# Performance work log

Measured on AMD Instinct MI355X. Metric: run time of the kernel, lower is better.

The kernel has to match this reference:

```python
import jax, jax.numpy as jnp
import numpy as np

B, DIN, H1, H2 = 16384, 512, 256, 128
S, DC, DE, T, TE, GH = 4, 4, 2, 3, 2, 64
NDOM = DC * DE            # 8 domain experts total
ETOT = S + NDOM + TE      # 14 experts feeding each task gate


def setup_inputs() -> dict:
    key = jax.random.key(0)
    ks = jax.random.split(key, 20)
    w = lambda k, shape, fan: (jax.random.normal(k, shape, jnp.float32) / np.sqrt(fan).astype(np.float32))
    x = jax.random.normal(ks[0], (B, DIN), jnp.float32)
    domain_ids = jax.random.randint(ks[1], (B,), 0, DC, jnp.int64) if jax.config.jax_enable_x64 else jax.random.randint(ks[1], (B,), 0, DC, jnp.int32)
    return {
        "x": x,
        "domain_ids": domain_ids,
        # shared experts (stacked): input->256->128, ReLU on both layers
        "sW1": w(ks[2], (S, DIN, H1), DIN), "sb1": jnp.zeros((S, H1), jnp.float32),
        "sW2": w(ks[3], (S, H1, H2), H1),   "sb2": jnp.zeros((S, H2), jnp.float32),
        # domain experts, all domains stacked in order domain0..domainDC-1
        "dW1": w(ks[4], (NDOM, DIN, H1), DIN), "db1": jnp.zeros((NDOM, H1), jnp.float32),
        "dW2": w(ks[5], (NDOM, H1, H2), H1),   "db2": jnp.zeros((NDOM, H2), jnp.float32),
        # task experts, all tasks stacked task0..taskT-1
        "tW1": w(ks[6], (T * TE, DIN, H1), DIN), "tb1": jnp.zeros((T * TE, H1), jnp.float32),
        "tW2": w(ks[7], (T * TE, H1, H2), H1),   "tb2": jnp.zeros((T * TE, H2), jnp.float32),
        # task gates (stacked over tasks): input->64 (ReLU) -> ETOT (linear) -> softmax
        "gW1": w(ks[8], (T, DIN, GH), DIN), "gb1": jnp.zeros((T, GH), jnp.float32),
        "gW2": w(ks[9], (T, GH, ETOT), GH), "gb2": jnp.zeros((T, ETOT), jnp.float32),
    }


def _experts(x, W1, b1, W2, b2):
    # x: [B, DIN]; W1: [E, DIN, H1]; W2: [E, H1, H2] -> [B, E, H2]
    h = jax.nn.relu(jnp.einsum('bi,eih->beh', x, W1) + b1)
    return jax.nn.relu(jnp.einsum('beh,eho->beo', h, W2) + b2)


def reference(x, domain_ids, sW1, sb1, sW2, sb2, dW1, db1, dW2, db2,
              tW1, tb1, tW2, tb2, gW1, gb1, gW2, gb2):
    shared = _experts(x, sW1, sb1, sW2, sb2)          # [B, S, H2]
    domain = _experts(x, dW1, db1, dW2, db2)          # [B, NDOM, H2]
    task = _experts(x, tW1, tb1, tW2, tb2)            # [B, T*TE, H2]
    task = task.reshape(B, T, TE, H2)
    base = jnp.concatenate([shared, domain], axis=1)  # [B, S+NDOM, H2]
    base = jnp.broadcast_to(base[:, None], (B, T, S + NDOM, H2))
    all_experts = jnp.concatenate([base, task], axis=2)  # [B, T, ETOT, H2]
    # task gates
    gh = jax.nn.relu(jnp.einsum('bi,tig->btg', x, gW1) + gb1)
    gates = jax.nn.softmax(jnp.einsum('btg,tge->bte', gh, gW2) + gb2, axis=-1)  # [B, T, ETOT]
    out = jnp.einsum('bteh,bte->tbh', all_experts, gates)  # [T, B, H2]
    # note: the torch per-sample domain_weighted_output is computed then discarded;
    # only these task outputs are returned, and they do not depend on domain_ids.
    return tuple(out[t] for t in range(T))
```

## Files before the change

### kernel.cpp

```cpp
#include <hip/hip_runtime.h>
#include <hip/hip_bf16.h>

#define NB 16384
#define DIN 512
#define H1 256
#define H2 128
#define NE 18
#define NT 3
#define NGH 64
#define NETOT 14

typedef float f32x4 __attribute__((ext_vector_type(4)));
typedef short s16x8 __attribute__((ext_vector_type(8)));
typedef unsigned short u16;
typedef unsigned int u32;

__device__ __forceinline__ u16 f2bf(float f) {
    union { float f; u32 u; } v; v.f = f;
    u32 r = v.u + 0x7fffu + ((v.u >> 16) & 1u);
    return (u16)(r >> 16);
}
__device__ __forceinline__ float bf2f(u16 u) {
    union { u32 u; float f; } v; v.u = ((u32)u) << 16;
    return v.f;
}
__device__ __forceinline__ u32 cvtpk(float a, float b) {
    u32 r;
    asm("v_cvt_pk_bf16_f32 %0, %1, %2" : "=v"(r) : "v"(a), "v"(b));
    return r;
}

#define GLDS16(g, l) __builtin_amdgcn_global_load_lds((const u32*)(g), (u32*)(l), 16, 0, 0)

__global__ __launch_bounds__(256) void k_prep(
    const float* __restrict__ x, u16* __restrict__ xb,
    const float* __restrict__ sW1, const float* __restrict__ dW1, const float* __restrict__ tW1,
    const float* __restrict__ sW2, const float* __restrict__ dW2, const float* __restrict__ tW2,
    const float* __restrict__ gW1, u16* __restrict__ w1t, u16* __restrict__ w2t, u16* __restrict__ gw1t)
{
    __shared__ float lds[64 * 65];
    int bx = blockIdx.x;
    if (bx < 8192) {
        int i = (bx * 256 + threadIdx.x) * 4;
        float4 v = *reinterpret_cast<const float4*>(x + i);
        ushort4 o;
        o.x = f2bf(v.x); o.y = f2bf(v.y); o.z = f2bf(v.z); o.w = f2bf(v.w);
        *reinterpret_cast<ushort4*>(xb + i) = o;
        return;
    }
    int b = bx - 8192;
    const float* src; u16* dst; int K, N, k0, n0;
    if (b < 576) {
        int e = b >> 5, tile = b & 31;
        src = (e < 4) ? sW1 + (size_t)e * DIN * H1 : (e < 12) ? dW1 + (size_t)(e - 4) * DIN * H1
                                                              : tW1 + (size_t)(e - 12) * DIN * H1;
        dst = w1t + (size_t)e * H1 * DIN; K = DIN; N = H1;
        k0 = (tile >> 2) * 64; n0 = (tile & 3) * 64;
    } else if (b < 720) {
        int b2 = b - 576; int e = b2 >> 3, tile = b2 & 7;
        src = (e < 4) ? sW2 + (size_t)e * H1 * H2 : (e < 12) ? dW2 + (size_t)(e - 4) * H1 * H2
                                                             : tW2 + (size_t)(e - 12) * H1 * H2;
        dst = w2t + (size_t)e * H2 * H1; K = H1; N = H2;
        k0 = (tile >> 1) * 64; n0 = (tile & 1) * 64;
    } else {
        int b3 = b - 720; int t = b3 >> 3, tile = b3 & 7;
        src = gW1 + (size_t)t * DIN * NGH; dst = gw1t + (size_t)t * NGH * DIN; K = DIN; N = NGH;
        k0 = tile * 64; n0 = 0;
    }
    int t = threadIdx.x;
#pragma unroll
    for (int i = 0; i < 16; ++i) {
        int idx = i * 256 + t;
        int kk = idx >> 6, nn = idx & 63;
        lds[kk * 65 + nn] = src[(size_t)(k0 + kk) * N + n0 + nn];
    }
    __syncthreads();
#pragma unroll
    for (int i = 0; i < 16; ++i) {
        int idx = i * 256 + t;
        int nn = idx >> 6, kk = idx & 63;
        dst[(size_t)(n0 + nn) * K + k0 + kk] = f2bf(lds[kk * 65 + nn]);
    }
}

__global__ __launch_bounds__(256, 2) void k_expert_gate(
    const u16* __restrict__ xb, const u16* __restrict__ w1t, const u16* __restrict__ w2t,
    const float* __restrict__ sb1, const float* __restrict__ db1, const float* __restrict__ tb1,
    const float* __restrict__ sb2, const float* __restrict__ db2, const float* __restrict__ tb2,
    u16* __restrict__ eout,
    const u16* __restrict__ gw1t, const float* __restrict__ gb1,
    const float* __restrict__ gw2, const float* __restrict__ gb2, float* __restrict__ gates)
{
    __shared__ __align__(128) char smem[73728];

    const int bid = blockIdx.x;
    const int tid = threadIdx.x;

    if (bid >= 2304) {
        u16* xs  = reinterpret_cast<u16*>(smem);
        u16* g1s = reinterpret_cast<u16*>(smem) + 4608;
        float* ghs = reinterpret_cast<float*>(smem);

        int m0 = (bid - 2304) * 64;
        int w = tid >> 6, lane = tid & 63;
        int wm = w & 1, wn = w >> 1;
        int l15 = lane & 15, lk = (lane >> 4) * 8, lr4 = (lane >> 4) * 4;

        f32x4 acc[2][6];
#pragma unroll
        for (int i = 0; i < 2; ++i)
#pragma unroll
            for (int j = 0; j < 6; ++j) acc[i][j] = (f32x4)0.f;

        const u16* xg = xb + (size_t)m0 * DIN;
        int srow = tid >> 3, su = (tid & 7) * 8;
        for (int kc = 0; kc < DIN / 64; ++kc) {
#pragma unroll
            for (int it = 0; it < 2; ++it) {
                int rr = srow + it * 32;
                *reinterpret_cast<uint4*>(&xs[rr * 72 + su]) =
                    *reinterpret_cast<const uint4*>(xg + (size_t)rr * DIN + kc * 64 + su);
            }
#pragma unroll
            for (int it = 0; it < 6; ++it) {
                int rr = srow + it * 32;
                *reinterpret_cast<uint4*>(&g1s[rr * 72 + su]) =
                    *reinterpret_cast<const uint4*>(gw1t + (size_t)rr * DIN + kc * 64 + su);
            }
            __syncthreads();
            s16x8 af[2][2], bfr[6][2];
#pragma unroll
            for (int mi = 0; mi < 2; ++mi)
#pragma unroll
                for (int kk = 0; kk < 2; ++kk)
                    af[mi][kk] = *reinterpret_cast<const s16x8*>(&xs[(wm * 32 + mi * 16 + l15) * 72 + kk * 32 + lk]);
#pragma unroll
            for (int nj = 0; nj < 6; ++nj)
#pragma unroll
                for (int kk = 0; kk < 2; ++kk)
                    bfr[nj][kk] = *reinterpret_cast<const s16x8*>(&g1s[(wn * 96 + nj * 16 + l15) * 72 + kk * 32 + lk]);
#pragma unroll
            for (int kk = 0; kk < 2; ++kk)
#pragma unroll
                for (int mi = 0; mi < 2; ++mi)
#pragma unroll
                    for (int nj = 0; nj < 6; ++nj)
                        acc[mi][nj] = __builtin_amdgcn_mfma_f32_16x16x32_bf16(af[mi][kk], bfr[nj][kk], acc[mi][nj], 0, 0, 0);
            __syncthreads();
        }
#pragma unroll
        for (int mi = 0; mi < 2; ++mi)
#pragma unroll
            for (int nj = 0; nj < 6; ++nj) {
                int col = wn * 96 + nj * 16 + l15;
                float bias = gb1[col];
#pragma unroll
                for (int r = 0; r < 4; ++r) {
                    int row = wm * 32 + mi * 16 + lr4 + r;
                    float v = acc[mi][nj][r] + bias;
                    ghs[row * 200 + col] = v > 0.f ? v : 0.f;
                }
            }
        __syncthreads();

        if (tid < 192) {
            int tt = tid >> 6, rr = tid & 63;
            float logit[NETOT];
#pragma unroll
            for (int e2 = 0; e2 < NETOT; ++e2) logit[e2] = gb2[tt * NETOT + e2];
            const float* g2 = gw2 + tt * NGH * NETOT;
            const float* gr = &ghs[rr * 200 + tt * 64];
            for (int g = 0; g < NGH; ++g) {
                float v = gr[g];
#pragma unroll
                for (int e2 = 0; e2 < NETOT; ++e2) logit[e2] += v * g2[g * NETOT + e2];
            }
            float m = logit[0];
#pragma unroll
            for (int e2 = 1; e2 < NETOT; ++e2) m = fmaxf(m, logit[e2]);
            float s = 0.f, p[NETOT];
#pragma unroll
            for (int e2 = 0; e2 < NETOT; ++e2) { p[e2] = __expf(logit[e2] - m); s += p[e2]; }
            float inv = 1.f / s;
            float* go = gates + (size_t)(m0 + rr) * (NT * NETOT) + tt * NETOT;
#pragma unroll
            for (int e2 = 0; e2 < NETOT; ++e2) go[e2] = p[e2] * inv;
        }
        return;
    }

    const int e  = bid >> 7;
    const int m0 = (bid & 127) * 128;
    const int w = tid >> 6, lane = tid & 63;
    const int l15 = lane & 15, q = lane >> 4;
    const int q16 = q * 16;
    const int swk = ((l15 >> 1) & 3) << 4;

    const u16* xg  = xb + (size_t)m0 * DIN;
    const u16* w1g = w1t + (size_t)e * H1 * DIN;
    const u16* w2g = w2t + (size_t)e * H2 * H1;
    const float* b1p = (e < 4) ? sb1 + e * H1 : (e < 12) ? db1 + (e - 4) * H1 : tb1 + (e - 12) * H1;
    const float* b2p = (e < 4) ? sb2 + e * H2 : (e < 12) ? db2 + (e - 4) * H2 : tb2 + (e - 12) * H2;

    const int sr = lane >> 2, sc = lane & 3;
    const u16* gx[2]; int lx[2];
#pragma unroll
    for (int j = 0; j < 2; ++j) {
        int row = w * 32 + j * 16 + sr;
        gx[j] = xg + (size_t)row * DIN + ((sc ^ ((row >> 1) & 3)) * 8);
        lx[j] = w * 2048 + j * 1024;
    }
    const u16* gw1[4]; int lw1[4];
#pragma unroll
    for (int j = 0; j < 4; ++j) {
        int row = w * 64 + j * 16 + sr;
        gw1[j] = w1g + (size_t)row * DIN + ((sc ^ ((row >> 1) & 3)) * 8);
        lw1[j] = 8192 + w * 4096 + j * 1024;
    }

    int offX[8], offW[4];
#pragma unroll
    for (int mi = 0; mi < 8; ++mi)
        offX[mi] = (mi * 16 + l15) * 64 + (q16 ^ swk);
#pragma unroll
    for (int nj = 0; nj < 4; ++nj)
        offW[nj] = 8192 + (w * 64 + nj * 16 + l15) * 64 + (q16 ^ swk);

    f32x4 acc1[8][4];
#pragma unroll
    for (int i = 0; i < 8; ++i)
#pragma unroll
        for (int j = 0; j < 4; ++j) acc1[i][j] = (f32x4)0.f;

#pragma unroll
    for (int j = 0; j < 2; ++j) GLDS16(gx[j], smem + lx[j]);
#pragma unroll
    for (int j = 0; j < 4; ++j) GLDS16(gw1[j], smem + lw1[j]);
#pragma unroll
    for (int j = 0; j < 2; ++j) GLDS16(gx[j] + 32, smem + 24576 + lx[j]);
#pragma unroll
    for (int j = 0; j < 4; ++j) GLDS16(gw1[j] + 32, smem + 24576 + lw1[j]);

    int cur = 0, stg = 2;
    for (int kt = 0; kt < 16; ++kt) {
        if (kt < 15) {
            asm volatile("s_waitcnt vmcnt(6)" ::: "memory");
        } else {
            asm volatile("s_waitcnt vmcnt(0)" ::: "memory");
        }
        __builtin_amdgcn_s_barrier();

        if (kt < 14) {
            const int sb = stg * 24576, ko = (kt + 2) * 32;
#pragma unroll
            for (int j = 0; j < 2; ++j) GLDS16(gx[j] + ko, smem + sb + lx[j]);
#pragma unroll
            for (int j = 0; j < 4; ++j) GLDS16(gw1[j] + ko, smem + sb + lw1[j]);
        }

        const char* cb = smem + cur * 24576;
        s16x8 xf[8], wf[4];
#pragma unroll
        for (int nj = 0; nj < 4; ++nj) wf[nj] = *(const s16x8*)(cb + offW[nj]);
#pragma unroll
        for (int mi = 0; mi < 8; ++mi) xf[mi] = *(const s16x8*)(cb + offX[mi]);
        __builtin_amdgcn_s_setprio(1);
#pragma unroll
        for (int mi = 0; mi < 8; ++mi)
#pragma unroll
            for (int nj = 0; nj < 4; ++nj)
                acc1[mi][nj] = __builtin_amdgcn_mfma_f32_16x16x32_bf16(wf[nj], xf[mi], acc1[mi][nj], 0, 0, 0);
        __builtin_amdgcn_s_setprio(0);

        cur = (cur == 2) ? 0 : cur + 1;
        stg = (stg == 2) ? 0 : stg + 1;
    }
    __syncthreads();

#pragma unroll
    for (int mi = 0; mi < 8; ++mi) {
        const int m = mi * 16 + l15;
        char* rowp = smem + m * 528;
#pragma unroll
        for (int nj = 0; nj < 4; ++nj) {
            const int n0 = w * 64 + nj * 16 + q * 4;
            const float4 bv = *reinterpret_cast<const float4*>(b1p + n0);
            float v0 = fmaxf(acc1[mi][nj][0] + bv.x, 0.f);
            float v1 = fmaxf(acc1[mi][nj][1] + bv.y, 0.f);
            float v2 = fmaxf(acc1[mi][nj][2] + bv.z, 0.f);
            float v3 = fmaxf(acc1[mi][nj][3] + bv.w, 0.f);
            uint2 hv; hv.x = cvtpk(v0, v1); hv.y = cvtpk(v2, v3);
            *reinterpret_cast<uint2*>(rowp + n0 * 2) = hv;
        }
    }
    __syncthreads();

    f32x4 acc2[8][2];
#pragma unroll
    for (int i = 0; i < 8; ++i)
#pragma unroll
        for (int j = 0; j < 2; ++j) acc2[i][j] = (f32x4)0.f;
    const u16* w2p0 = w2g + (size_t)(w * 32 + l15) * H1 + q * 8;
    const u16* w2p1 = w2g + (size_t)(w * 32 + 16 + l15) * H1 + q * 8;
#pragma unroll
    for (int kt2 = 0; kt2 < 8; ++kt2) {
        s16x8 wf2[2], hf[8];
        wf2[0] = *(const s16x8*)(w2p0 + kt2 * 32);
        wf2[1] = *(const s16x8*)(w2p1 + kt2 * 32);
#pragma unroll
        for (int mi = 0; mi < 8; ++mi)
            hf[mi] = *(const s16x8*)(smem + (mi * 16 + l15) * 528 + kt2 * 64 + q16);
#pragma unroll
        for (int mi = 0; mi < 8; ++mi)
#pragma unroll
            for (int pj = 0; pj < 2; ++pj)
                acc2[mi][pj] = __builtin_amdgcn_mfma_f32_16x16x32_bf16(hf[mi], wf2[pj], acc2[mi][pj], 0, 0, 0);
    }

    u16* eo = eout + ((size_t)e * NB + m0) * H2;
#pragma unroll
    for (int mi = 0; mi < 8; ++mi)
#pragma unroll
        for (int pj = 0; pj < 2; ++pj) {
            const int p = w * 32 + pj * 16 + l15;
            const float bias = b2p[p];
#pragma unroll
            for (int r = 0; r < 4; ++r) {
                const int row = mi * 16 + q * 4 + r;
                float v = acc2[mi][pj][r] + bias;
                eo[(size_t)row * H2 + p] = f2bf(v > 0.f ? v : 0.f);
            }
        }
}

__global__ __launch_bounds__(256) void k_combine(
    const u16* __restrict__ eout, const float* __restrict__ gates, float* __restrict__ out)
{
    int tid = threadIdx.x;
    int lr = tid >> 5, hq = tid & 31;
    int b = blockIdx.x * 8 + lr;
    int h0 = hq * 4;
    const float* g = gates + (size_t)b * (NT * NETOT);
    float o0[4] = {0, 0, 0, 0}, o1[4] = {0, 0, 0, 0}, o2[4] = {0, 0, 0, 0};
#pragma unroll
    for (int e = 0; e < NE; ++e) {
        ushort4 ev = *reinterpret_cast<const ushort4*>(&eout[((size_t)e * NB + b) * H2 + h0]);
        float v0 = bf2f(ev.x), v1 = bf2f(ev.y), v2 = bf2f(ev.z), v3 = bf2f(ev.w);
        if (e < 12) {
            float wa = g[e], wb = g[NETOT + e], wc = g[2 * NETOT + e];
            o0[0] += wa * v0; o0[1] += wa * v1; o0[2] += wa * v2; o0[3] += wa * v3;
            o1[0] += wb * v0; o1[1] += wb * v1; o1[2] += wb * v2; o1[3] += wb * v3;
            o2[0] += wc * v0; o2[1] += wc * v1; o2[2] += wc * v2; o2[3] += wc * v3;
        } else {
            int t = (e - 12) >> 1, te = (e - 12) & 1;
            float wt = g[t * NETOT + 12 + te];
            float* ot = (t == 0) ? o0 : (t == 1) ? o1 : o2;
            ot[0] += wt * v0; ot[1] += wt * v1; ot[2] += wt * v2; ot[3] += wt * v3;
        }
    }
    size_t base = (size_t)b * H2 + h0;
    *reinterpret_cast<float4*>(&out[0 * (size_t)NB * H2 + base]) = make_float4(o0[0], o0[1], o0[2], o0[3]);
    *reinterpret_cast<float4*>(&out[1 * (size_t)NB * H2 + base]) = make_float4(o1[0], o1[1], o1[2], o1[3]);
    *reinterpret_cast<float4*>(&out[2 * (size_t)NB * H2 + base]) = make_float4(o2[0], o2[1], o2[2], o2[3]);
}

extern "C" void kernel_launch(void* const* d_in, const int* in_sizes, int n_in,
                              void* d_out, int out_size, void* d_ws, size_t ws_size,
                              hipStream_t stream)
{
    const float* x   = (const float*)d_in[0];
    const float* sW1 = (const float*)d_in[2];
    const float* sb1 = (const float*)d_in[3];
    const float* sW2 = (const float*)d_in[4];
    const float* sb2 = (const float*)d_in[5];
    const float* dW1 = (const float*)d_in[6];
    const float* db1 = (const float*)d_in[7];
    const float* dW2 = (const float*)d_in[8];
    const float* db2 = (const float*)d_in[9];
    const float* tW1 = (const float*)d_in[10];
    const float* tb1 = (const float*)d_in[11];
    const float* tW2 = (const float*)d_in[12];
    const float* tb2 = (const float*)d_in[13];
    const float* gW1 = (const float*)d_in[14];
    const float* gb1 = (const float*)d_in[15];
    const float* gW2 = (const float*)d_in[16];
    const float* gb2 = (const float*)d_in[17];

    char* ws = (char*)d_ws;
    u16*  xb    = (u16*)(ws + 0);
    u16*  w1t   = (u16*)(ws + 16777216);
    u16*  w2t   = (u16*)(ws + 21495808);
    u16*  gw1t  = (u16*)(ws + 22675456);
    float* gates = (float*)(ws + 22872064);
    u16*  eout  = (u16*)(ws + 25624576);

    k_prep<<<dim3(8936), dim3(256), 0, stream>>>(x, xb, sW1, dW1, tW1, sW2, dW2, tW2, gW1, w1t, w2t, gw1t);
    k_expert_gate<<<dim3(2560), dim3(256), 0, stream>>>(xb, w1t, w2t, sb1, db1, tb1, sb2, db2, tb2,
                                                        eout, gw1t, gb1, gW2, gb2, gates);
    k_combine<<<dim3(NB / 8), dim3(256), 0, stream>>>(eout, gates, (float*)d_out);
}
```

Baseline: 147.9 us.

## Enlarge expert tile to 256 rows with 512-thread blocks and double buffering

The expert GEMM block grows from 128 to 256 batch rows and from 4 to 8 waves in a 2x4 layout, so each expert weight tile loaded into LDS serves twice as many rows. The K loop switches from a 3-stage, 32-wide pipeline to a 2-stage, 64-wide double buffer with an XOR swizzle and a full vmcnt(0) wait plus barrier each step. The gate path is adapted so only 4 of the 8 waves compute. In exchange, LDS use rises to about 132KB, which allows one block per CU, and the extra barriers and full drains may expose load latency.

Measured after the change: 152.5 us. 3.1% more time.

```diff
diff --git a/kernel.cpp b/kernel.cpp
--- a/kernel.cpp
+++ b/kernel.cpp
@@ -31,6 +31,7 @@
 }
 
 #define GLDS16(g, l) __builtin_amdgcn_global_load_lds((const u32*)(g), (u32*)(l), 16, 0, 0)
+#define VMCNT0_BARRIER() do { asm volatile("s_waitcnt vmcnt(0)" ::: "memory"); __builtin_amdgcn_s_barrier(); } while (0)
 
 __global__ __launch_bounds__(256) void k_prep(
     const float* __restrict__ x, u16* __restrict__ xb,
@@ -83,7 +84,7 @@
     }
 }
 
-__global__ __launch_bounds__(256, 2) void k_expert_gate(
+__global__ __launch_bounds__(512, 1) void k_expert_gate(
     const u16* __restrict__ xb, const u16* __restrict__ w1t, const u16* __restrict__ w2t,
     const float* __restrict__ sb1, const float* __restrict__ db1, const float* __restrict__ tb1,
     const float* __restrict__ sb2, const float* __restrict__ db2, const float* __restrict__ tb2,
@@ -91,20 +92,22 @@
     const u16* __restrict__ gw1t, const float* __restrict__ gb1,
     const float* __restrict__ gw2, const float* __restrict__ gb2, float* __restrict__ gates)
 {
-    __shared__ __align__(128) char smem[73728];
+    __shared__ __align__(128) char smem[135168];
 
     const int bid = blockIdx.x;
     const int tid = threadIdx.x;
-
-    if (bid >= 2304) {
+    const int w = tid >> 6, lane = tid & 63;
+    const int l15 = lane & 15, q = lane >> 4;
+    const int q16 = q * 16;
+
+    if (bid >= 1152) {
         u16* xs  = reinterpret_cast<u16*>(smem);
         u16* g1s = reinterpret_cast<u16*>(smem) + 4608;
         float* ghs = reinterpret_cast<float*>(smem);
 
-        int m0 = (bid - 2304) * 64;
-        int w = tid >> 6, lane = tid & 63;
-        int wm = w & 1, wn = w >> 1;
-        int l15 = lane & 15, lk = (lane >> 4) * 8, lr4 = (lane >> 4) * 4;
+        int m0 = (bid - 1152) * 64;
+        int wm = w & 1, wn = (w >> 1) & 1;
+        int lk = q * 8, lr4 = q * 4;
 
         f32x4 acc[2][6];
 #pragma unroll
@@ -113,54 +116,54 @@
             for (int j = 0; j < 6; ++j) acc[i][j] = (f32x4)0.f;
 
         const u16* xg = xb + (size_t)m0 * DIN;
-        int srow = tid >> 3, su = (tid & 7) * 8;
+        const int srow = tid >> 3, su = (tid & 7) * 8;
         for (int kc = 0; kc < DIN / 64; ++kc) {
-#pragma unroll
-            for (int it = 0; it < 2; ++it) {
-                int rr = srow + it * 32;
-                *reinterpret_cast<uint4*>(&xs[rr * 72 + su]) =
-                    *reinterpret_cast<const uint4*>(xg + (size_t)rr * DIN + kc * 64 + su);
-            }
-#pragma unroll
-            for (int it = 0; it < 6; ++it) {
-                int rr = srow + it * 32;
+            *reinterpret_cast<uint4*>(&xs[srow * 72 + su]) =
+                *reinterpret_cast<const uint4*>(xg + (size_t)srow * DIN + kc * 64 + su);
+#pragma unroll
+            for (int it = 0; it < 3; ++it) {
+                int rr = it * 64 + srow;
                 *reinterpret_cast<uint4*>(&g1s[rr * 72 + su]) =
                     *reinterpret_cast<const uint4*>(gw1t + (size_t)rr * DIN + kc * 64 + su);
             }
             __syncthreads();
-            s16x8 af[2][2], bfr[6][2];
+            if (w < 4) {
+                s16x8 af[2][2], bfr[6][2];
+#pragma unroll
+                for (int mi = 0; mi < 2; ++mi)
+#pragma unroll
+                    for (int kk = 0; kk < 2; ++kk)
+                        af[mi][kk] = *reinterpret_cast<const s16x8*>(&xs[(wm * 32 + mi * 16 + l15) * 72 + kk * 32 + lk]);
+#pragma unroll
+                for (int nj = 0; nj < 6; ++nj)
+#pragma unroll
+                    for (int kk = 0; kk < 2; ++kk)
+                        bfr[nj][kk] = *reinterpret_cast<const s16x8*>(&g1s[(wn * 96 + nj * 16 + l15) * 72 + kk * 32 + lk]);
+#pragma unroll
+                for (int kk = 0; kk < 2; ++kk)
+#pragma unroll
+                    for (int mi = 0; mi < 2; ++mi)
+#pragma unroll
+                        for (int nj = 0; nj < 6; ++nj)
+                            acc[mi][nj] = __builtin_amdgcn_mfma_f32_16x16x32_bf16(af[mi][kk], bfr[nj][kk], acc[mi][nj], 0, 0, 0);
+            }
+            __syncthreads();
+        }
+        if (w < 4) {
 #pragma unroll
             for (int mi = 0; mi < 2; ++mi)
 #pragma unroll
-                for (int kk = 0; kk < 2; ++kk)
-                    af[mi][kk] = *reinterpret_cast<const s16x8*>(&xs[(wm * 32 + mi * 16 + l15) * 72 + kk * 32 + lk]);
-#pragma unroll
-            for (int nj = 0; nj < 6; ++nj)
-#pragma unroll
-                for (int kk = 0; kk < 2; ++kk)
-                    bfr[nj][kk] = *reinterpret_cast<const s16x8*>(&g1s[(wn * 96 + nj * 16 + l15) * 72 + kk * 32 + lk]);
-#pragma unroll
-            for (int kk = 0; kk < 2; ++kk)
-#pragma unroll
-                for (int mi = 0; mi < 2; ++mi)
-#pragma unroll
-                    for (int nj = 0; nj < 6; ++nj)
-                        acc[mi][nj] = __builtin_amdgcn_mfma_f32_16x16x32_bf16(af[mi][kk], bfr[nj][kk], acc[mi][nj], 0, 0, 0);
-            __syncthreads();
-        }
-#pragma unroll
-        for (int mi = 0; mi < 2; ++mi)
-#pragma unroll
-            for (int nj = 0; nj < 6; ++nj) {
-                int col = wn * 96 + nj * 16 + l15;
-                float bias = gb1[col];
-#pragma unroll
-                for (int r = 0; r < 4; ++r) {
-                    int row = wm * 32 + mi * 16 + lr4 + r;
-                    float v = acc[mi][nj][r] + bias;
-                    ghs[row * 200 + col] = v > 0.f ? v : 0.f;
+                for (int nj = 0; nj < 6; ++nj) {
+                    int col = wn * 96 + nj * 16 + l15;
+                    float bias = gb1[col];
+#pragma unroll
+                    for (int r = 0; r < 4; ++r) {
+                        int row = wm * 32 + mi * 16 + lr4 + r;
+                        float v = acc[mi][nj][r] + bias;
+                        ghs[row * 200 + col] = v > 0.f ? v : 0.f;
+                    }
                 }
-            }
+        }
         __syncthreads();
 
         if (tid < 192) {
@@ -189,12 +192,9 @@
         return;
     }
 
-    const int e  = bid >> 7;
-    const int m0 = (bid & 127) * 128;
-    const int w = tid >> 6, lane = tid & 63;
-    const int l15 = lane & 15, q = lane >> 4;
-    const int q16 = q * 16;
-    const int swk = ((l15 >> 1) & 3) << 4;
+    const int e  = bid >> 6;
+    const int m0 = (bid & 63) * 256;
+    const int wm = w >> 2, wn = w & 3;
 
     const u16* xg  = xb + (size_t)m0 * DIN;
     const u16* w1g = w1t + (size_t)e * H1 * DIN;
@@ -202,29 +202,28 @@
     const float* b1p = (e < 4) ? sb1 + e * H1 : (e < 12) ? db1 + (e - 4) * H1 : tb1 + (e - 12) * H1;
     const float* b2p = (e < 4) ? sb2 + e * H2 : (e < 12) ? db2 + (e - 4) * H2 : tb2 + (e - 12) * H2;
 
-    const int sr = lane >> 2, sc = lane & 3;
-    const u16* gx[2]; int lx[2];
-#pragma unroll
-    for (int j = 0; j < 2; ++j) {
-        int row = w * 32 + j * 16 + sr;
-        gx[j] = xg + (size_t)row * DIN + ((sc ^ ((row >> 1) & 3)) * 8);
-        lx[j] = w * 2048 + j * 1024;
-    }
-    const u16* gw1[4]; int lw1[4];
+    const int srow8 = lane >> 3, sslot = lane & 7;
+    const u16* gxa[4]; const u16* gxb[4]; int lxa[4], lxb[4];
 #pragma unroll
     for (int j = 0; j < 4; ++j) {
-        int row = w * 64 + j * 16 + sr;
-        gw1[j] = w1g + (size_t)row * DIN + ((sc ^ ((row >> 1) & 3)) * 8);
-        lw1[j] = 8192 + w * 4096 + j * 1024;
-    }
-
-    int offX[8], offW[4];
-#pragma unroll
-    for (int mi = 0; mi < 8; ++mi)
-        offX[mi] = (mi * 16 + l15) * 64 + (q16 ^ swk);
-#pragma unroll
-    for (int nj = 0; nj < 4; ++nj)
-        offW[nj] = 8192 + (w * 64 + nj * 16 + l15) * 64 + (q16 ^ swk);
+        int baserow = w * 32 + j * 8, row = baserow + srow8;
+        gxa[j] = xg  + (size_t)row * DIN + ((sslot ^ (row & 7)) * 8);
+        gxb[j] = w1g + (size_t)row * DIN + ((sslot ^ (row & 7)) * 8);
+        lxa[j] = baserow * 128;
+        lxb[j] = 65536 + baserow * 128;
+    }
+
+    int offX[8], swA[8], offW[4], swB[4];
+#pragma unroll
+    for (int mi = 0; mi < 8; ++mi) {
+        int r = wm * 128 + mi * 16 + l15;
+        offX[mi] = r * 128; swA[mi] = (r & 7) << 4;
+    }
+#pragma unroll
+    for (int nj = 0; nj < 4; ++nj) {
+        int n = wn * 64 + nj * 16 + l15;
+        offW[nj] = 65536 + n * 128; swB[nj] = (n & 7) << 4;
+    }
 
     f32x4 acc1[8][4];
 #pragma unroll
@@ -233,57 +232,68 @@
         for (int j = 0; j < 4; ++j) acc1[i][j] = (f32x4)0.f;
 
 #pragma unroll
-    for (int j = 0; j < 2; ++j) GLDS16(gx[j], smem + lx[j]);
-#pragma unroll
-    for (int j = 0; j < 4; ++j) GLDS16(gw1[j], smem + lw1[j]);
-#pragma unroll
-    for (int j = 0; j < 2; ++j) GLDS16(gx[j] + 32, smem + 24576 + lx[j]);
-#pragma unroll
-    for (int j = 0; j < 4; ++j) GLDS16(gw1[j] + 32, smem + 24576 + lw1[j]);
-
-    int cur = 0, stg = 2;
-    for (int kt = 0; kt < 16; ++kt) {
-        if (kt < 15) {
-            asm volatile("s_waitcnt vmcnt(6)" ::: "memory");
-        } else {
-            asm volatile("s_waitcnt vmcnt(0)" ::: "memory");
-        }
-        __builtin_amdgcn_s_barrier();
-
-        if (kt < 14) {
-            const int sb = stg * 24576, ko = (kt + 2) * 32;
-#pragma unroll
-            for (int j = 0; j < 2; ++j) GLDS16(gx[j] + ko, smem + sb + lx[j]);
-#pragma unroll
-            for (int j = 0; j < 4; ++j) GLDS16(gw1[j] + ko, smem + sb + lw1[j]);
-        }
-
-        const char* cb = smem + cur * 24576;
-        s16x8 xf[8], wf[4];
-#pragma unroll
-        for (int nj = 0; nj < 4; ++nj) wf[nj] = *(const s16x8*)(cb + offW[nj]);
-#pragma unroll
-        for (int mi = 0; mi < 8; ++mi) xf[mi] = *(const s16x8*)(cb + offX[mi]);
-        __builtin_amdgcn_s_setprio(1);
-#pragma unroll
-        for (int mi = 0; mi < 8; ++mi)
+    for (int j = 0; j < 4; ++j) GLDS16(gxa[j], smem + lxa[j]);
+#pragma unroll
+    for (int j = 0; j < 4; ++j) GLDS16(gxb[j], smem + lxb[j]);
+
+    int buf = 0;
+    for (int kt = 0; kt < 8; ++kt) {
+        VMCNT0_BARRIER();
+        if (kt < 7) {
+            const int nb = (buf ^ 1) * 32768, ko = (kt + 1) * 64;
+#pragma unroll
+            for (int j = 0; j < 4; ++j) GLDS16(gxa[j] + ko, smem + nb + lxa[j]);
+#pragma unroll
+            for (int j = 0; j < 4; ++j) GLDS16(gxb[j] + ko, smem + nb + lxb[j]);
+        }
+        const int cb = buf * 32768;
+#pragma unroll
+        for (int kk = 0; kk < 2; ++kk) {
+            const int kb = kk * 64 + q16;
+            s16x8 wf[4];
 #pragma unroll
             for (int nj = 0; nj < 4; ++nj)
-                acc1[mi][nj] = __builtin_amdgcn_mfma_f32_16x16x32_bf16(wf[nj], xf[mi], acc1[mi][nj], 0, 0, 0);
-        __builtin_amdgcn_s_setprio(0);
-
-        cur = (cur == 2) ? 0 : cur + 1;
-        stg = (stg == 2) ? 0 : stg + 1;
+                wf[nj] = *(const s16x8*)(smem + cb + offW[nj] + (kb ^ swB[nj]));
+            {
+                s16x8 xf[4];
+#pragma unroll
+                for (int i = 0; i < 4; ++i)
+                    xf[i] = *(const s16x8*)(smem + cb + offX[i] + (kb ^ swA[i]));
+                __builtin_amdgcn_s_setprio(1);
+#pragma unroll
+                for (int i = 0; i < 4; ++i)
+#pragma unroll
+                    for (int nj = 0; nj < 4; ++nj)
+                        acc1[i][nj] = __builtin_amdgcn_mfma_f32_16x16x32_bf16(wf[nj], xf[i], acc1[i][nj], 0, 0, 0);
+                __builtin_amdgcn_s_setprio(0);
+            }
+            __builtin_amdgcn_s_barrier();
+            {
+                s16x8 xf[4];
+#pragma unroll
+                for (int i = 0; i < 4; ++i)
+                    xf[i] = *(const s16x8*)(smem + cb + offX[4 + i] + (kb ^ swA[4 + i]));
+                __builtin_amdgcn_s_setprio(1);
+#pragma unroll
+                for (int i = 0; i < 4; ++i)
+#pragma unroll
+                    for (int nj = 0; nj < 4; ++nj)
+                        acc1[4 + i][nj] = __builtin_amdgcn_mfma_f32_16x16x32_bf16(wf[nj], xf[i], acc1[4 + i][nj], 0, 0, 0);
+                __builtin_amdgcn_s_setprio(0);
+            }
+            if (kk == 0) __builtin_amdgcn_s_barrier();
+        }
+        buf ^= 1;
     }
     __syncthreads();
 
 #pragma unroll
     for (int mi = 0; mi < 8; ++mi) {
-        const int m = mi * 16 + l15;
+        const int m = wm * 128 + mi * 16 + l15;
         char* rowp = smem + m * 528;
 #pragma unroll
         for (int nj = 0; nj < 4; ++nj) {
-            const int n0 = w * 64 + nj * 16 + q * 4;
+            const int n0 = wn * 64 + nj * 16 + q * 4;
             const float4 bv = *reinterpret_cast<const float4*>(b1p + n0);
             float v0 = fmaxf(acc1[mi][nj][0] + bv.x, 0.f);
             float v1 = fmaxf(acc1[mi][nj][1] + bv.y, 0.f);
@@ -300,8 +310,8 @@
     for (int i = 0; i < 8; ++i)
 #pragma unroll
         for (int j = 0; j < 2; ++j) acc2[i][j] = (f32x4)0.f;
-    const u16* w2p0 = w2g + (size_t)(w * 32 + l15) * H1 + q * 8;
-    const u16* w2p1 = w2g + (size_t)(w * 32 + 16 + l15) * H1 + q * 8;
+    const u16* w2p0 = w2g + (size_t)(wn * 32 + l15) * H1 + q * 8;
+    const u16* w2p1 = w2g + (size_t)(wn * 32 + 16 + l15) * H1 + q * 8;
 #pragma unroll
     for (int kt2 = 0; kt2 < 8; ++kt2) {
         s16x8 wf2[2], hf[8];
@@ -309,7 +319,7 @@
         wf2[1] = *(const s16x8*)(w2p1 + kt2 * 32);
 #pragma unroll
         for (int mi = 0; mi < 8; ++mi)
-            hf[mi] = *(const s16x8*)(smem + (mi * 16 + l15) * 528 + kt2 * 64 + q16);
+            hf[mi] = *(const s16x8*)(smem + (wm * 128 + mi * 16 + l15) * 528 + kt2 * 64 + q16);
 #pragma unroll
         for (int mi = 0; mi < 8; ++mi)
 #pragma unroll
@@ -322,11 +332,11 @@
     for (int mi = 0; mi < 8; ++mi)
 #pragma unroll
         for (int pj = 0; pj < 2; ++pj) {
-            const int p = w * 32 + pj * 16 + l15;
+            const int p = wn * 32 + pj * 16 + l15;
             const float bias = b2p[p];
 #pragma unroll
             for (int r = 0; r < 4; ++r) {
-                const int row = mi * 16 + q * 4 + r;
+                const int row = wm * 128 + mi * 16 + q * 4 + r;
                 float v = acc2[mi][pj][r] + bias;
                 eo[(size_t)row * H2 + p] = f2bf(v > 0.f ? v : 0.f);
             }
@@ -395,7 +405,7 @@
     u16*  eout  = (u16*)(ws + 25624576);
 
     k_prep<<<dim3(8936), dim3(256), 0, stream>>>(x, xb, sW1, dW1, tW1, sW2, dW2, tW2, gW1, w1t, w2t, gw1t);
-    k_expert_gate<<<dim3(2560), dim3(256), 0, stream>>>(xb, w1t, w2t, sb1, db1, tb1, sb2, db2, tb2,
+    k_expert_gate<<<dim3(1408), dim3(512), 0, stream>>>(xb, w1t, w2t, sb1, db1, tb1, sb2, db2, tb2,
                                                         eout, gw1t, gb1, gW2, gb2, gates);
     k_combine<<<dim3(NB / 8), dim3(256), 0, stream>>>(eout, gates, (float*)d_out);
 }
```

## Switch expert MLP kernel from 16x16x32 to 32x32x16 bf16 MFMA tiles

Applied to the files above, without the earlier changes.

Rewrites both GEMM stages of the expert kernel to use 32x32x16 MFMA instructions with 16-wide accumulators instead of 16x16x32. It changes the LDS fragment offsets and swizzle, the hidden-layer staging stride (528 to 536 bytes), and the epilogue index mapping to match the new output layout. The aim is fewer LDS reads per FLOP and higher MFMA throughput from the larger tile. In exchange, the new layout may cause LDS bank conflicts, and the second-layer output stores are strided per element. Some leftover no-op statements remain in the store loop.

Result: slower. 157.3 us (+6.4%).

```diff
diff --git a/kernel.cpp b/kernel.cpp
--- a/kernel.cpp
+++ b/kernel.cpp
@@ -11,6 +11,7 @@
 #define NETOT 14
 
 typedef float f32x4 __attribute__((ext_vector_type(4)));
+typedef float f32x16 __attribute__((ext_vector_type(16)));
 typedef short s16x8 __attribute__((ext_vector_type(8)));
 typedef unsigned short u16;
 typedef unsigned int u32;
@@ -192,9 +193,10 @@
     const int e  = bid >> 7;
     const int m0 = (bid & 127) * 128;
     const int w = tid >> 6, lane = tid & 63;
-    const int l15 = lane & 15, q = lane >> 4;
-    const int q16 = q * 16;
-    const int swk = ((l15 >> 1) & 3) << 4;
+    const int l31 = lane & 31;
+    const int hh  = lane >> 5;
+    const int h16 = hh << 4;
+    const int h4  = hh << 2;
 
     const u16* xg  = xb + (size_t)m0 * DIN;
     const u16* w1g = w1t + (size_t)e * H1 * DIN;
@@ -218,19 +220,29 @@
         lw1[j] = 8192 + w * 4096 + j * 1024;
     }
 
-    int offX[8], offW[4];
-#pragma unroll
-    for (int mi = 0; mi < 8; ++mi)
-        offX[mi] = (mi * 16 + l15) * 64 + (q16 ^ swk);
-#pragma unroll
-    for (int nj = 0; nj < 4; ++nj)
-        offW[nj] = 8192 + (w * 64 + nj * 16 + l15) * 64 + (q16 ^ swk);
-
-    f32x4 acc1[8][4];
-#pragma unroll
-    for (int i = 0; i < 8; ++i)
-#pragma unroll
-        for (int j = 0; j < 4; ++j) acc1[i][j] = (f32x4)0.f;
+    int oX[4][2], oW[2][2];
+#pragma unroll
+    for (int mi = 0; mi < 4; ++mi) {
+        int r = mi * 32 + l31;
+        int sw = ((r >> 1) & 3) << 4;
+#pragma unroll
+        for (int kk = 0; kk < 2; ++kk)
+            oX[mi][kk] = r * 64 + ((kk * 32 + h16) ^ sw);
+    }
+#pragma unroll
+    for (int nj = 0; nj < 2; ++nj) {
+        int n = w * 64 + nj * 32 + l31;
+        int sw = ((n >> 1) & 3) << 4;
+#pragma unroll
+        for (int kk = 0; kk < 2; ++kk)
+            oW[nj][kk] = 8192 + n * 64 + ((kk * 32 + h16) ^ sw);
+    }
+
+    f32x16 acc1[4][2];
+#pragma unroll
+    for (int i = 0; i < 4; ++i)
+#pragma unroll
+        for (int j = 0; j < 2; ++j) acc1[i][j] = (f32x16)0.f;
 
 #pragma unroll
     for (int j = 0; j < 2; ++j) GLDS16(gx[j], smem + lx[j]);
@@ -259,17 +271,25 @@
         }
 
         const char* cb = smem + cur * 24576;
-        s16x8 xf[8], wf[4];
-#pragma unroll
-        for (int nj = 0; nj < 4; ++nj) wf[nj] = *(const s16x8*)(cb + offW[nj]);
-#pragma unroll
-        for (int mi = 0; mi < 8; ++mi) xf[mi] = *(const s16x8*)(cb + offX[mi]);
+        s16x8 xf[4][2], wf[2][2];
+#pragma unroll
+        for (int nj = 0; nj < 2; ++nj)
+#pragma unroll
+            for (int kk = 0; kk < 2; ++kk)
+                wf[nj][kk] = *(const s16x8*)(cb + oW[nj][kk]);
+#pragma unroll
+        for (int mi = 0; mi < 4; ++mi)
+#pragma unroll
+            for (int kk = 0; kk < 2; ++kk)
+                xf[mi][kk] = *(const s16x8*)(cb + oX[mi][kk]);
         __builtin_amdgcn_s_setprio(1);
 #pragma unroll
-        for (int mi = 0; mi < 8; ++mi)
-#pragma unroll
-            for (int nj = 0; nj < 4; ++nj)
-                acc1[mi][nj] = __builtin_amdgcn_mfma_f32_16x16x32_bf16(wf[nj], xf[mi], acc1[mi][nj], 0, 0, 0);
+        for (int kk = 0; kk < 2; ++kk)
+#pragma unroll
+            for (int mi = 0; mi < 4; ++mi)
+#pragma unroll
+                for (int nj = 0; nj < 2; ++nj)
+                    acc1[mi][nj] = __builtin_amdgcn_mfma_f32_32x32x16_bf16(wf[nj][kk], xf[mi][kk], acc1[mi][nj], 0, 0, 0);
         __builtin_amdgcn_s_setprio(0);
 
         cur = (cur == 2) ? 0 : cur + 1;
@@ -278,59 +298,58 @@
     __syncthreads();
 
 #pragma unroll
-    for (int mi = 0; mi < 8; ++mi) {
-        const int m = mi * 16 + l15;
-        char* rowp = smem + m * 528;
-#pragma unroll
-        for (int nj = 0; nj < 4; ++nj) {
-            const int n0 = w * 64 + nj * 16 + q * 4;
-            const float4 bv = *reinterpret_cast<const float4*>(b1p + n0);
-            float v0 = fmaxf(acc1[mi][nj][0] + bv.x, 0.f);
-            float v1 = fmaxf(acc1[mi][nj][1] + bv.y, 0.f);
-            float v2 = fmaxf(acc1[mi][nj][2] + bv.z, 0.f);
-            float v3 = fmaxf(acc1[mi][nj][3] + bv.w, 0.f);
-            uint2 hv; hv.x = cvtpk(v0, v1); hv.y = cvtpk(v2, v3);
-            *reinterpret_cast<uint2*>(rowp + n0 * 2) = hv;
+    for (int mi = 0; mi < 4; ++mi) {
+        const int m = mi * 32 + l31;
+        char* rowp = smem + m * 536;
+#pragma unroll
+        for (int nj = 0; nj < 2; ++nj) {
+#pragma unroll
+            for (int rq = 0; rq < 4; ++rq) {
+                const int n0 = w * 64 + nj * 32 + rq * 8 + h4;
+                const float4 bv = *reinterpret_cast<const float4*>(b1p + n0);
+                float v0 = fmaxf(acc1[mi][nj][rq * 4 + 0] + bv.x, 0.f);
+                float v1 = fmaxf(acc1[mi][nj][rq * 4 + 1] + bv.y, 0.f);
+                float v2 = fmaxf(acc1[mi][nj][rq * 4 + 2] + bv.z, 0.f);
+                float v3 = fmaxf(acc1[mi][nj][rq * 4 + 3] + bv.w, 0.f);
+                uint2 hv; hv.x = cvtpk(v0, v1); hv.y = cvtpk(v2, v3);
+                *reinterpret_cast<uint2*>(rowp + n0 * 2) = hv;
+            }
         }
     }
     __syncthreads();
 
-    f32x4 acc2[8][2];
-#pragma unroll
-    for (int i = 0; i < 8; ++i)
-#pragma unroll
-        for (int j = 0; j < 2; ++j) acc2[i][j] = (f32x4)0.f;
-    const u16* w2p0 = w2g + (size_t)(w * 32 + l15) * H1 + q * 8;
-    const u16* w2p1 = w2g + (size_t)(w * 32 + 16 + l15) * H1 + q * 8;
-#pragma unroll
-    for (int kt2 = 0; kt2 < 8; ++kt2) {
-        s16x8 wf2[2], hf[8];
-        wf2[0] = *(const s16x8*)(w2p0 + kt2 * 32);
-        wf2[1] = *(const s16x8*)(w2p1 + kt2 * 32);
-#pragma unroll
-        for (int mi = 0; mi < 8; ++mi)
-            hf[mi] = *(const s16x8*)(smem + (mi * 16 + l15) * 528 + kt2 * 64 + q16);
-#pragma unroll
-        for (int mi = 0; mi < 8; ++mi)
-#pragma unroll
-            for (int pj = 0; pj < 2; ++pj)
-                acc2[mi][pj] = __builtin_amdgcn_mfma_f32_16x16x32_bf16(hf[mi], wf2[pj], acc2[mi][pj], 0, 0, 0);
-    }
-
-    u16* eo = eout + ((size_t)e * NB + m0) * H2;
-#pragma unroll
-    for (int mi = 0; mi < 8; ++mi)
-#pragma unroll
-        for (int pj = 0; pj < 2; ++pj) {
-            const int p = w * 32 + pj * 16 + l15;
-            const float bias = b2p[p];
-#pragma unroll
-            for (int r = 0; r < 4; ++r) {
-                const int row = mi * 16 + q * 4 + r;
-                float v = acc2[mi][pj][r] + bias;
-                eo[(size_t)row * H2 + p] = f2bf(v > 0.f ? v : 0.f);
-            }
-        }
+    f32x16 acc2[4];
+#pragma unroll
+    for (int i = 0; i < 4; ++i) acc2[i] = (f32x16)0.f;
+    const u16* w2p = w2g + (size_t)(w * 32 + l31) * H1 + hh * 8;
+    const float bias2 = b2p[w * 32 + l31];
+#pragma unroll
+    for (int s = 0; s < 16; ++s) {
+        s16x8 wf2 = *(const s16x8*)(w2p + s * 16);
+        s16x8 hf[4];
+#pragma unroll
+        for (int mi = 0; mi < 4; ++mi)
+            hf[mi] = *(const s16x8*)(smem + (mi * 32 + l31) * 536 + s * 32 + h16);
+#pragma unroll
+        for (int mi = 0; mi < 4; ++mi)
+            acc2[mi] = __builtin_amdgcn_mfma_f32_32x32x16_bf16(hf[mi], wf2, acc2[mi], 0, 0, 0);
+    }
+
+    u16* eo = eout + ((size_t)e * NB + m0) * H2 + (w * 32 + l31);
+#pragma unroll
+    for (int mi = 0; mi < 4; ++mi)
+#pragma unroll
+        for (int rq = 0; rq < 4; ++rq)
+#pragma unroll
+            for (int j = 0; j < 4; ++j) {
+                const int row = mi * 32 + rq * 8 + h4 + j;
+                float v = acc2[mi][rq * 4 + j] + bias2;
+                eo[(size_t)row * H2] = f2bf(v > 0.f ? v : 0.f);
+                if (0) {}
+                ;
+                (void)0;
+                continue;
+            }
 }
 
 __global__ __launch_bounds__(256) void k_combine(
```
